# Performance work log

Hardware: AMD Instinct MI355X
Metric: run time of the kernel (lower is better)

The kernel has to match this reference:

```python
import jax, jax.numpy as jnp
import numpy as np

B, L, V, E_ENC, D_DEC, E_EMB = 256, 128, 4096, 1024, 1024, 512


def _lin(key, out_f, in_f, scale=0.02):
    k1, k2 = jax.random.split(key)
    return (jax.random.normal(k1, (out_f, in_f), jnp.float32) * scale,
            jax.random.normal(k2, (out_f,), jnp.float32) * scale)


def setup_inputs() -> dict:
    key = jax.random.key(0)
    ks = jax.random.split(key, 12)
    x = jax.random.normal(ks[0], (B, 1, V), jnp.float32)
    hidden = jax.random.normal(ks[1], (1, B, D_DEC), jnp.float32)
    enc_output = jax.random.normal(ks[2], (B, L, E_ENC), jnp.float32)
    W1_w, W1_b = _lin(ks[3], D_DEC, E_ENC)
    W2_w, W2_b = _lin(ks[4], D_DEC, D_DEC)
    V_w, V_b = _lin(ks[5], 1, D_DEC)
    out2emb_w, out2emb_b = _lin(ks[6], E_EMB, V)
    gru_wi, gru_bi = _lin(ks[7], 3 * D_DEC, E_EMB + E_ENC)
    gru_wh, gru_bh = _lin(ks[8], 3 * D_DEC, D_DEC)
    fc1_w, fc1_b = _lin(ks[9], E_EMB, D_DEC)
    fc2_w, fc2_b = _lin(ks[10], V, E_EMB)
    return dict(x=x, hidden=hidden, enc_output=enc_output,
                W1_w=W1_w, W1_b=W1_b, W2_w=W2_w, W2_b=W2_b, V_w=V_w, V_b=V_b,
                out2emb_w=out2emb_w, out2emb_b=out2emb_b,
                gru_wi=gru_wi, gru_wh=gru_wh, gru_bi=gru_bi, gru_bh=gru_bh,
                fc1_w=fc1_w, fc1_b=fc1_b, fc2_w=fc2_w, fc2_b=fc2_b)


def reference(x, hidden, enc_output, W1_w, W1_b, W2_w, W2_b, V_w, V_b,
              out2emb_w, out2emb_b, gru_wi, gru_wh, gru_bi, gru_bh,
              fc1_w, fc1_b, fc2_w, fc2_b):
    # --- Bahdanau additive attention ---
    h_t = hidden[-1][:, None, :]                                   # (B,1,dec)
    score = jnp.tanh(enc_output @ W1_w.T + W1_b + h_t @ W2_w.T + W2_b)  # (B,L,dec)
    attn = jax.nn.softmax(score @ V_w.T + V_b, axis=1)             # (B,L,1)
    context = jnp.sum(attn * enc_output, axis=1)                   # (B,enc)
    # --- embed previous output distribution ---
    x_emb = x @ out2emb_w.T + out2emb_b                            # (B,1,emb)
    rnn_in = jnp.concatenate([context[:, None, :], x_emb], -1)[:, 0, :]  # (B,emb+enc)
    # --- single GRU step (PyTorch gate layout r,z,n) ---
    h0 = hidden[0]
    gi = rnn_in @ gru_wi.T + gru_bi
    gh = h0 @ gru_wh.T + gru_bh
    ir, iz, inn = jnp.split(gi, 3, axis=-1)
    hr, hz, hn = jnp.split(gh, 3, axis=-1)
    r = jax.nn.sigmoid(ir + hr)
    z = jax.nn.sigmoid(iz + hz)
    n = jnp.tanh(inn + r * hn)
    h_new = (1.0 - z) * n + z * h0                                 # (B,dec)
    # --- output MLP ---
    out = jnp.tanh(h_new @ fc1_w.T + fc1_b) @ fc2_w.T + fc2_b      # (B,vocab)
    return out, h_new[None], attn
```

## Files before the change

kernel.cpp:

```cpp
#include <hip/hip_runtime.h>
#include <math.h>


#define B_   256
#define L_   128
#define V_   4096
#define ENC_ 1024
#define DEC_ 1024
#define EMB_ 512
#define MB_  1048576ull

typedef __bf16 bf16;
typedef __bf16 bf16x8 __attribute__((ext_vector_type(8)));
typedef __bf16 bf16x4 __attribute__((ext_vector_type(4)));
typedef float  f32x4  __attribute__((ext_vector_type(4)));

__device__ __forceinline__ float fast_tanh(float x) {
  float e = __builtin_amdgcn_exp2f(x * 2.88539008177792681472f);
  return 1.0f - 2.0f * __builtin_amdgcn_rcpf(e + 1.0f);
}
__device__ __forceinline__ float fast_sigmoid(float x) {
  return __builtin_amdgcn_rcpf(1.0f + __builtin_amdgcn_exp2f(-1.44269504088896f * x));
}

__device__ __forceinline__ void cp16(const void* g, void* l) {
  __builtin_amdgcn_global_load_lds(
      (const __attribute__((address_space(1))) void*)g,
      (__attribute__((address_space(3))) void*)l,
      16, 0, 0);
}

__device__ __forceinline__ bf16x8 ld8f(const float* f) {
  f32x4 a = *(const f32x4*)f;
  f32x4 b = *(const f32x4*)(f + 4);
  bf16x8 r;
  r[0] = (bf16)a[0]; r[1] = (bf16)a[1]; r[2] = (bf16)a[2]; r[3] = (bf16)a[3];
  r[4] = (bf16)b[0]; r[5] = (bf16)b[1]; r[6] = (bf16)b[2]; r[7] = (bf16)b[3];
  return r;
}


__device__ __forceinline__ void gemm64_f32(
    const float* __restrict__ A, const float* __restrict__ Brow,
    int strideA, int strideB, int kbeg, int kend, int row0,
    bf16* As, bf16* Bs, f32x4 acc[4])
{
  const int t   = threadIdx.x;
  const int lane = t & 63, w = t >> 6, q = lane >> 4, c16 = lane & 15;
  const int sr  = t >> 3, lb = t & 7;

  for (int k0 = kbeg; k0 < kend; k0 += 64) {
    bf16x8 va[2], vb[2];
#pragma unroll
    for (int ch = 0; ch < 2; ch++) {
      int r    = ch * 32 + sr;
      int gcol = k0 + ((lb ^ (r & 7)) << 3);
      va[ch] = ld8f(A    + (size_t)(row0 + r) * strideA + gcol);
      vb[ch] = ld8f(Brow + (size_t)r * strideB + gcol);
    }
#pragma unroll
    for (int ch = 0; ch < 2; ch++) {
      *(bf16x8*)&As[ch * 2048 + t * 8] = va[ch];
      *(bf16x8*)&Bs[ch * 2048 + t * 8] = vb[ch];
    }
    __syncthreads();
#pragma unroll
    for (int kkb = 0; kkb < 8; kkb += 4) {
      int rb = w * 16 + c16;
      bf16x8 bfr = *(const bf16x8*)&Bs[rb * 64 + (((kkb + q) ^ (rb & 7)) << 3)];
#pragma unroll
      for (int i = 0; i < 4; i++) {
        int ra = i * 16 + c16;
        bf16x8 af = *(const bf16x8*)&As[ra * 64 + (((kkb + q) ^ (ra & 7)) << 3)];
        acc[i] = __builtin_amdgcn_mfma_f32_16x16x32_bf16(af, bfr, acc[i], 0, 0, 0);
      }
    }
    __syncthreads();
  }
}

__global__ __launch_bounds__(256) void setup_k(
    const float* __restrict__ hidden, const float* __restrict__ W2,
    const float* __restrict__ wh, const float* __restrict__ W1_b,
    const float* __restrict__ W2_b, const float* __restrict__ gbh,
    const float* __restrict__ x, const float* __restrict__ o2e,
    const float* __restrict__ enc, const float* __restrict__ W1,
    const float* __restrict__ wi, const float* __restrict__ fc1w,
    const float* __restrict__ fc2w,
    bf16* __restrict__ enc_bf, bf16* __restrict__ W1_bf,
    bf16* __restrict__ wi_bf, bf16* __restrict__ fc1_bf,
    bf16* __restrict__ fc2_bf,
    bf16* __restrict__ u, bf16* __restrict__ gh, float* __restrict__ xe4)
{
  __shared__ __align__(16) bf16 As[64 * 64];
  __shared__ __align__(16) bf16 Bs[64 * 64];

  const int bid = blockIdx.x;
  const int t   = threadIdx.x;

  if (bid >= 384) {
    int i = bid - 384;
    const float* src; bf16* dst; int blk;
    if      (i < 8192) { src = enc;  dst = enc_bf; blk = i; }
    else if (i < 8448) { src = W1;   dst = W1_bf;  blk = i - 8192; }
    else if (i < 9600) { src = wi;   dst = wi_bf;  blk = i - 8448; }
    else if (i < 9728) { src = fc1w; dst = fc1_bf; blk = i - 9600; }
    else               { src = fc2w; dst = fc2_bf; blk = i - 9728; }
    const size_t base = (size_t)blk * 4096 + t * 16;
    const float* s = src + base;
    bf16* d = dst + base;
    *(bf16x8*)(d)     = ld8f(s);
    *(bf16x8*)(d + 8) = ld8f(s + 8);
    return;
  }

  const int lane = t & 63, w = t >> 6, q = lane >> 4, c16 = lane & 15;
  f32x4 acc[4] = {};

  if (bid < 256) {
    const int row0 = (bid >> 6) * 64;
    const int col0 = (bid & 63) * 64;
    const bool isU = (col0 < 1024);
    const float* Brow = isU ? (W2 + (size_t)col0 * 1024)
                            : (wh + (size_t)(col0 - 1024) * 1024);
    gemm64_f32(hidden, Brow, 1024, 1024, 0, 1024, row0, As, Bs, acc);

    const int gc = col0 + w * 16 + c16;
    float bias = isU ? (W1_b[gc] + W2_b[gc]) : gbh[gc - 1024];
#pragma unroll
    for (int i = 0; i < 4; i++) {
      int gr0 = row0 + i * 16 + q * 4;
#pragma unroll
      for (int r = 0; r < 4; r++) {
        float v = acc[i][r] + bias;
        if (isU) u[(size_t)(gr0 + r) * 1024 + gc] = (bf16)v;
        else     gh[(size_t)(gr0 + r) * 3072 + (gc - 1024)] = (bf16)v;
      }
    }
  } else {
    const int i3   = bid - 256;
    const int col0 = (i3 & 7) * 64;
    const int row0 = ((i3 >> 3) & 3) * 64;
    const int z    = i3 >> 5;
    gemm64_f32(x, o2e + (size_t)col0 * 4096, 4096, 4096,
               z * 1024, z * 1024 + 1024, row0, As, Bs, acc);

    const int gc = col0 + w * 16 + c16;
    float* out = xe4 + (size_t)z * 131072;
#pragma unroll
    for (int i = 0; i < 4; i++) {
      int gr0 = row0 + i * 16 + q * 4;
#pragma unroll
      for (int r = 0; r < 4; r++)
        out[(size_t)(gr0 + r) * 512 + gc] = acc[i][r];
    }
  }
}

__global__ __launch_bounds__(256) void score_f2(
    const bf16* __restrict__ A,
    const bf16* __restrict__ Bw,
    const bf16* __restrict__ u,
    const float* __restrict__ Vw,
    float* __restrict__ e_part)
{
  __shared__ __align__(16) bf16 As[128 * 64];
  __shared__ __align__(16) bf16 Bs[128 * 64];
  __shared__ float s_part[2][128];

  const int t    = threadIdx.x;
  const int lane = t & 63;
  const int w    = t >> 6;
  const int wm   = w >> 1;
  const int wn   = w & 1;
  const int q    = lane >> 4;
  const int c16  = lane & 15;
  const int sr   = t >> 3;
  const int lb   = t & 7;

  const int row0 = blockIdx.y * 128;
  const int b    = blockIdx.y;

  float rowsum[4][4] = {};

#pragma unroll 1
  for (int cbp = 0; cbp < 2; cbp++) {
    const int col0 = (blockIdx.x * 2 + cbp) * 128;
    f32x4 acc[4][4] = {};

    for (int k0 = 0; k0 < 1024; k0 += 64) {
#pragma unroll
      for (int ch = 0; ch < 4; ch++) {
        int r    = ch * 32 + sr;
        int gcol = k0 + ((lb ^ (r & 7)) << 3);
        cp16(A  + (size_t)(row0 + r) * 1024 + gcol, &As[ch * 2048 + t * 8]);
        cp16(Bw + (size_t)(col0 + r) * 1024 + gcol, &Bs[ch * 2048 + t * 8]);
      }
      __syncthreads();
#pragma unroll
      for (int kkb = 0; kkb < 8; kkb += 4) {
        bf16x8 af[4], bfr[4];
#pragma unroll
        for (int i = 0; i < 4; i++) {
          int ra = wm * 64 + i * 16 + c16;
          af[i] = *(const bf16x8*)&As[ra * 64 + (((kkb + q) ^ (ra & 7)) << 3)];
        }
#pragma unroll
        for (int j = 0; j < 4; j++) {
          int rb = wn * 64 + j * 16 + c16;
          bfr[j] = *(const bf16x8*)&Bs[rb * 64 + (((kkb + q) ^ (rb & 7)) << 3)];
        }
#pragma unroll
        for (int i = 0; i < 4; i++)
#pragma unroll
          for (int j = 0; j < 4; j++)
            acc[i][j] = __builtin_amdgcn_mfma_f32_16x16x32_bf16(af[i], bfr[j], acc[i][j], 0, 0, 0);
      }
      __syncthreads();
    }

#pragma unroll
    for (int i = 0; i < 4; i++) {
#pragma unroll
      for (int j = 0; j < 4; j++) {
        int gc   = col0 + wn * 64 + j * 16 + c16;
        float uc = (float)u[b * 1024 + gc];
        float vw = Vw[gc];
#pragma unroll
        for (int r = 0; r < 4; r++)
          rowsum[i][r] += fast_tanh(acc[i][j][r] + uc) * vw;
      }
    }
  }

#pragma unroll
  for (int i = 0; i < 4; i++) {
#pragma unroll
    for (int r = 0; r < 4; r++) {
      float v = rowsum[i][r];
      v += __shfl_xor(v, 1);
      v += __shfl_xor(v, 2);
      v += __shfl_xor(v, 4);
      v += __shfl_xor(v, 8);
      if (c16 == 0) s_part[wn][wm * 64 + i * 16 + q * 4 + r] = v;
    }
  }
  __syncthreads();
  if (t < 128)
    e_part[(size_t)blockIdx.x * 32768 + row0 + t] = s_part[0][t] + s_part[1][t];
}

__global__ __launch_bounds__(256) void softmax_f(
    const float* __restrict__ e_part,
    const bf16* __restrict__ enc,
    const float* __restrict__ xe4,
    const float* __restrict__ o2eb,
    float* __restrict__ attn_out,
    bf16* __restrict__ rnn_in)
{
  const int b = blockIdx.x;
  const int t = threadIdx.x;
  __shared__ float se[128];

  if (t < 128) {
    float s = 0.0f;
#pragma unroll
    for (int cb = 0; cb < 4; cb++) s += e_part[(size_t)cb * 32768 + b * 128 + t];
    se[t] = s;
  }
  __syncthreads();

  float m = -1e30f;
  for (int l = 0; l < 128; l++) m = fmaxf(m, se[l]);
  float sum = 0.0f;
  for (int l = 0; l < 128; l++) sum += expf(se[l] - m);
  float inv = 1.0f / sum;
  __syncthreads();
  if (t < 128) {
    float p = expf(se[t] - m) * inv;
    attn_out[b * 128 + t] = p;
    se[t] = p;
  }
  __syncthreads();

  float a0 = 0, a1 = 0, a2 = 0, a3 = 0;
  const bf16* ep = enc + (size_t)b * L_ * ENC_ + t * 4;
  for (int l = 0; l < 128; l++) {
    float p = se[l];
    bf16x4 v = *(const bf16x4*)(ep + (size_t)l * ENC_);
    a0 += p * (float)v[0]; a1 += p * (float)v[1];
    a2 += p * (float)v[2]; a3 += p * (float)v[3];
  }
  bf16x4 o;
  o[0] = (bf16)a0; o[1] = (bf16)a1; o[2] = (bf16)a2; o[3] = (bf16)a3;
  *(bf16x4*)(rnn_in + (size_t)b * 1536 + t * 4) = o;

#pragma unroll
  for (int jj = 0; jj < 2; jj++) {
    int j = jj * 256 + t;
    float v = o2eb[j];
#pragma unroll
    for (int z = 0; z < 4; z++) v += xe4[(size_t)z * 131072 + b * 512 + j];
    rnn_in[(size_t)b * 1536 + 1024 + j] = (bf16)v;
  }
}

template <int ACT, int OUTF32>
__global__ __launch_bounds__(256) void gemm_f(
    const bf16* __restrict__ A, const bf16* __restrict__ Bw,
    const float* __restrict__ bias1,
    void* __restrict__ C, int K, int out_ld)
{
  __shared__ __align__(16) bf16 As[64 * 64];
  __shared__ __align__(16) bf16 Bs[64 * 64];

  const int t    = threadIdx.x;
  const int lane = t & 63;
  const int w    = t >> 6;
  const int q    = lane >> 4;
  const int c16  = lane & 15;
  const int sr   = t >> 3;
  const int lb   = t & 7;
  const int row0 = blockIdx.y * 64;
  const int col0 = blockIdx.x * 64;

  f32x4 acc[4] = {};

  for (int k0 = 0; k0 < K; k0 += 64) {
#pragma unroll
    for (int ch = 0; ch < 2; ch++) {
      int r    = ch * 32 + sr;
      int gcol = k0 + ((lb ^ (r & 7)) << 3);
      cp16(A  + (size_t)(row0 + r) * K + gcol, &As[ch * 2048 + t * 8]);
      cp16(Bw + (size_t)(col0 + r) * K + gcol, &Bs[ch * 2048 + t * 8]);
    }
    __syncthreads();
#pragma unroll
    for (int kkb = 0; kkb < 8; kkb += 4) {
      int rb = w * 16 + c16;
      bf16x8 bfr = *(const bf16x8*)&Bs[rb * 64 + (((kkb + q) ^ (rb & 7)) << 3)];
#pragma unroll
      for (int i = 0; i < 4; i++) {
        int ra = i * 16 + c16;
        bf16x8 af = *(const bf16x8*)&As[ra * 64 + (((kkb + q) ^ (ra & 7)) << 3)];
        acc[i] = __builtin_amdgcn_mfma_f32_16x16x32_bf16(af, bfr, acc[i], 0, 0, 0);
      }
    }
    __syncthreads();
  }

  const int gc = col0 + w * 16 + c16;
  float bias = bias1[gc];
#pragma unroll
  for (int i = 0; i < 4; i++) {
    int gr0 = row0 + i * 16 + q * 4;
#pragma unroll
    for (int r = 0; r < 4; r++) {
      float v = acc[i][r] + bias;
      if (ACT == 1) v = fast_tanh(v);
      size_t off = (size_t)(gr0 + r) * out_ld + gc;
      if (OUTF32) ((float*)C)[off] = v;
      else        ((bf16*)C)[off] = (bf16)v;
    }
  }
}

__global__ __launch_bounds__(256) void gru_f(
    const bf16* __restrict__ gi, const bf16* __restrict__ gh,
    const float* __restrict__ h0,
    float* __restrict__ hnew_out, bf16* __restrict__ hnew_i)
{
  int idx = blockIdx.x * 256 + threadIdx.x;
  int b = idx >> 10, d = idx & 1023;
  const bf16* gib = gi + b * 3072;
  const bf16* ghb = gh + b * 3072;
  float ir = (float)gib[d], iz = (float)gib[1024 + d], in = (float)gib[2048 + d];
  float hr = (float)ghb[d], hz = (float)ghb[1024 + d], hn = (float)ghb[2048 + d];
  float r = fast_sigmoid(ir + hr);
  float z = fast_sigmoid(iz + hz);
  float n = fast_tanh(in + r * hn);
  float h = (1.0f - z) * n + z * h0[idx];
  hnew_out[idx] = h;
  hnew_i[idx]   = (bf16)h;
}

extern "C" void kernel_launch(void* const* d_in, const int* in_sizes, int n_in,
                              void* d_out, int out_size, void* d_ws, size_t ws_size,
                              hipStream_t stream) {
  const float* x      = (const float*)d_in[0];
  const float* hidden = (const float*)d_in[1];
  const float* enc    = (const float*)d_in[2];
  const float* W1_w   = (const float*)d_in[3];
  const float* W1_b   = (const float*)d_in[4];
  const float* W2_w   = (const float*)d_in[5];
  const float* W2_b   = (const float*)d_in[6];
  const float* V_w    = (const float*)d_in[7];
  const float* o2e_w  = (const float*)d_in[9];
  const float* o2e_b  = (const float*)d_in[10];
  const float* gru_wi = (const float*)d_in[11];
  const float* gru_wh = (const float*)d_in[12];
  const float* gru_bi = (const float*)d_in[13];
  const float* gru_bh = (const float*)d_in[14];
  const float* fc1_w  = (const float*)d_in[15];
  const float* fc1_b  = (const float*)d_in[16];
  const float* fc2_w  = (const float*)d_in[17];
  const float* fc2_b  = (const float*)d_in[18];

  float* out_main = (float*)d_out;
  float* out_h    = out_main + (size_t)B_ * V_;
  float* out_attn = out_h + (size_t)B_ * DEC_;

  char* ws = (char*)d_ws;
  bf16*  enc_bf  = (bf16*)(ws);
  bf16*  W1_bf   = (bf16*)(ws + 64 * MB_);
  bf16*  wi_bf   = (bf16*)(ws + 66 * MB_);
  bf16*  fc1_bf  = (bf16*)(ws + 75 * MB_);
  bf16*  fc2_bf  = (bf16*)(ws + 76 * MB_);
  bf16*  u_bf    = (bf16*)(ws + 80 * MB_);
  bf16*  gh_bf   = (bf16*)(ws + 80 * MB_ + 524288);
  float* e_part  = (float*)(ws + 82 * MB_);
  bf16*  gi_bf   = (bf16*)(ws + 82 * MB_ + 524288);
  bf16*  rnn_in  = (bf16*)(ws + 84 * MB_);
  bf16*  tbuf    = (bf16*)(ws + 84 * MB_ + 786432);
  bf16*  hnew_bf = (bf16*)(ws + 85 * MB_);
  float* xe4     = (float*)(ws + 85 * MB_ + 524288);

  setup_k<<<10624, 256, 0, stream>>>(
      hidden, W2_w, gru_wh, W1_b, W2_b, gru_bh, x, o2e_w,
      enc, W1_w, gru_wi, fc1_w, fc2_w,
      enc_bf, W1_bf, wi_bf, fc1_bf, fc2_bf, u_bf, gh_bf, xe4);

  score_f2<<<dim3(4, 256), 256, 0, stream>>>(enc_bf, W1_bf, u_bf, V_w, e_part);

  softmax_f<<<B_, 256, 0, stream>>>(e_part, enc_bf, xe4, o2e_b, out_attn, rnn_in);

  gemm_f<0, 0><<<dim3(48, 4), 256, 0, stream>>>(rnn_in, wi_bf, gru_bi, gi_bf, 1536, 3072);

  gru_f<<<(B_ * DEC_) / 256, 256, 0, stream>>>(gi_bf, gh_bf, hidden, out_h, hnew_bf);

  gemm_f<1, 0><<<dim3(8, 4), 256, 0, stream>>>(hnew_bf, fc1_bf, fc1_b, tbuf, 1024, 512);

  gemm_f<0, 1><<<dim3(64, 4), 256, 0, stream>>>(tbuf, fc2_bf, fc2_b, out_main, 512, 4096);
}
```

Baseline: 433.0 us.

## Fuse attention, softmax, GRU and output MLP into one persistent kernel with grid barriers

```diff
diff --git a/kernel.cpp b/kernel.cpp
--- a/kernel.cpp
+++ b/kernel.cpp
@@ -9,6 +9,7 @@
 #define DEC_ 1024
 #define EMB_ 512
 #define MB_  1048576ull
+#define NBLK 512
 
 typedef __bf16 bf16;
 typedef __bf16 bf16x8 __attribute__((ext_vector_type(8)));
@@ -39,16 +40,56 @@
   return r;
 }
 
+__device__ __forceinline__ void gbar(int* bar, int idx, int n) {
+  __syncthreads();
+  if (threadIdx.x == 0) {
+    __hip_atomic_fetch_add(&bar[idx], 1, __ATOMIC_ACQ_REL, __HIP_MEMORY_SCOPE_AGENT);
+    while (__hip_atomic_load(&bar[idx], __ATOMIC_ACQUIRE, __HIP_MEMORY_SCOPE_AGENT) < n)
+      __builtin_amdgcn_s_sleep(1);
+  }
+  __syncthreads();
+}
+
+
+__device__ __forceinline__ void gemm64_bf(
+    const bf16* __restrict__ A, const bf16* __restrict__ Bw, int K,
+    int row0, int col0, bf16* As, bf16* Bs, f32x4 acc[4])
+{
+  const int t = threadIdx.x;
+  const int lane = t & 63, w = t >> 6, q = lane >> 4, c16 = lane & 15;
+  const int sr = t >> 3, lb = t & 7;
+  for (int k0 = 0; k0 < K; k0 += 64) {
+#pragma unroll
+    for (int ch = 0; ch < 2; ch++) {
+      int r    = ch * 32 + sr;
+      int gcol = k0 + ((lb ^ (r & 7)) << 3);
+      cp16(A  + (size_t)(row0 + r) * K + gcol, &As[ch * 2048 + t * 8]);
+      cp16(Bw + (size_t)(col0 + r) * K + gcol, &Bs[ch * 2048 + t * 8]);
+    }
+    __syncthreads();
+#pragma unroll
+    for (int kkb = 0; kkb < 8; kkb += 4) {
+      int rb = w * 16 + c16;
+      bf16x8 bfr = *(const bf16x8*)&Bs[rb * 64 + (((kkb + q) ^ (rb & 7)) << 3)];
+#pragma unroll
+      for (int i = 0; i < 4; i++) {
+        int ra = i * 16 + c16;
+        bf16x8 af = *(const bf16x8*)&As[ra * 64 + (((kkb + q) ^ (ra & 7)) << 3)];
+        acc[i] = __builtin_amdgcn_mfma_f32_16x16x32_bf16(af, bfr, acc[i], 0, 0, 0);
+      }
+    }
+    __syncthreads();
+  }
+}
 
 __device__ __forceinline__ void gemm64_f32(
     const float* __restrict__ A, const float* __restrict__ Brow,
     int strideA, int strideB, int kbeg, int kend, int row0,
     bf16* As, bf16* Bs, f32x4 acc[4])
 {
-  const int t   = threadIdx.x;
+  const int t = threadIdx.x;
   const int lane = t & 63, w = t >> 6, q = lane >> 4, c16 = lane & 15;
-  const int sr  = t >> 3, lb = t & 7;
-
+  const int sr = t >> 3, lb = t & 7;
   for (int k0 = kbeg; k0 < kend; k0 += 64) {
     bf16x8 va[2], vb[2];
 #pragma unroll
@@ -157,17 +198,25 @@
   }
 }
 
-__global__ __launch_bounds__(256) void score_f2(
-    const bf16* __restrict__ A,
-    const bf16* __restrict__ Bw,
-    const bf16* __restrict__ u,
-    const float* __restrict__ Vw,
-    float* __restrict__ e_part)
+__global__ __launch_bounds__(256) void mega_k(
+    const bf16* __restrict__ enc_bf, const bf16* __restrict__ W1_bf,
+    const bf16* __restrict__ u_bf, const float* __restrict__ Vw,
+    float* __restrict__ e_part,
+    const float* __restrict__ xe4, const float* __restrict__ o2eb,
+    const bf16* __restrict__ wi_bf, const float* __restrict__ gru_bi,
+    const bf16* __restrict__ gh_bf, const float* __restrict__ h0,
+    const bf16* __restrict__ fc1_bf, const float* __restrict__ fc1_b,
+    const bf16* __restrict__ fc2_bf, const float* __restrict__ fc2_b,
+    bf16* __restrict__ rnn_in, bf16* __restrict__ gi_bf,
+    bf16* __restrict__ hnew_bf, bf16* __restrict__ tbuf,
+    float* __restrict__ attn_out, float* __restrict__ out_h,
+    float* __restrict__ out_main, int* __restrict__ bar)
 {
   __shared__ __align__(16) bf16 As[128 * 64];
   __shared__ __align__(16) bf16 Bs[128 * 64];
-  __shared__ float s_part[2][128];
-
+  __shared__ float s_misc[256];
+
+  const int bid  = blockIdx.x;
   const int t    = threadIdx.x;
   const int lane = t & 63;
   const int w    = t >> 6;
@@ -178,210 +227,193 @@
   const int sr   = t >> 3;
   const int lb   = t & 7;
 
-  const int row0 = blockIdx.y * 128;
-  const int b    = blockIdx.y;
-
-  float rowsum[4][4] = {};
+  {
+    const int b    = bid >> 1;
+    const int half = bid & 1;
+    const int row0 = b * 128;
+    float rowsum[4][4] = {};
 
 #pragma unroll 1
-  for (int cbp = 0; cbp < 2; cbp++) {
-    const int col0 = (blockIdx.x * 2 + cbp) * 128;
-    f32x4 acc[4][4] = {};
-
-    for (int k0 = 0; k0 < 1024; k0 += 64) {
-#pragma unroll
-      for (int ch = 0; ch < 4; ch++) {
-        int r    = ch * 32 + sr;
-        int gcol = k0 + ((lb ^ (r & 7)) << 3);
-        cp16(A  + (size_t)(row0 + r) * 1024 + gcol, &As[ch * 2048 + t * 8]);
-        cp16(Bw + (size_t)(col0 + r) * 1024 + gcol, &Bs[ch * 2048 + t * 8]);
+    for (int cb = half * 4; cb < half * 4 + 4; cb++) {
+      const int col0 = cb * 128;
+      f32x4 acc[4][4] = {};
+
+      for (int k0 = 0; k0 < 1024; k0 += 64) {
+#pragma unroll
+        for (int ch = 0; ch < 4; ch++) {
+          int r    = ch * 32 + sr;
+          int gcol = k0 + ((lb ^ (r & 7)) << 3);
+          cp16(enc_bf + (size_t)(row0 + r) * 1024 + gcol, &As[ch * 2048 + t * 8]);
+          cp16(W1_bf  + (size_t)(col0 + r) * 1024 + gcol, &Bs[ch * 2048 + t * 8]);
+        }
+        __syncthreads();
+#pragma unroll
+        for (int kkb = 0; kkb < 8; kkb += 4) {
+          bf16x8 af[4], bfr[4];
+#pragma unroll
+          for (int i = 0; i < 4; i++) {
+            int ra = wm * 64 + i * 16 + c16;
+            af[i] = *(const bf16x8*)&As[ra * 64 + (((kkb + q) ^ (ra & 7)) << 3)];
+          }
+#pragma unroll
+          for (int j = 0; j < 4; j++) {
+            int rb = wn * 64 + j * 16 + c16;
+            bfr[j] = *(const bf16x8*)&Bs[rb * 64 + (((kkb + q) ^ (rb & 7)) << 3)];
+          }
+#pragma unroll
+          for (int i = 0; i < 4; i++)
+#pragma unroll
+            for (int j = 0; j < 4; j++)
+              acc[i][j] = __builtin_amdgcn_mfma_f32_16x16x32_bf16(af[i], bfr[j], acc[i][j], 0, 0, 0);
+        }
+        __syncthreads();
       }
-      __syncthreads();
-#pragma unroll
-      for (int kkb = 0; kkb < 8; kkb += 4) {
-        bf16x8 af[4], bfr[4];
-#pragma unroll
-        for (int i = 0; i < 4; i++) {
-          int ra = wm * 64 + i * 16 + c16;
-          af[i] = *(const bf16x8*)&As[ra * 64 + (((kkb + q) ^ (ra & 7)) << 3)];
+
+#pragma unroll
+      for (int i = 0; i < 4; i++)
+#pragma unroll
+        for (int j = 0; j < 4; j++) {
+          int gc   = col0 + wn * 64 + j * 16 + c16;
+          float uc = (float)u_bf[b * 1024 + gc];
+          float vw = Vw[gc];
+#pragma unroll
+          for (int r = 0; r < 4; r++)
+            rowsum[i][r] += fast_tanh(acc[i][j][r] + uc) * vw;
         }
-#pragma unroll
-        for (int j = 0; j < 4; j++) {
-          int rb = wn * 64 + j * 16 + c16;
-          bfr[j] = *(const bf16x8*)&Bs[rb * 64 + (((kkb + q) ^ (rb & 7)) << 3)];
-        }
-#pragma unroll
-        for (int i = 0; i < 4; i++)
-#pragma unroll
-          for (int j = 0; j < 4; j++)
-            acc[i][j] = __builtin_amdgcn_mfma_f32_16x16x32_bf16(af[i], bfr[j], acc[i][j], 0, 0, 0);
+    }
+
+#pragma unroll
+    for (int i = 0; i < 4; i++)
+#pragma unroll
+      for (int r = 0; r < 4; r++) {
+        float v = rowsum[i][r];
+        v += __shfl_xor(v, 1);
+        v += __shfl_xor(v, 2);
+        v += __shfl_xor(v, 4);
+        v += __shfl_xor(v, 8);
+        if (c16 == 0) s_misc[wn * 128 + wm * 64 + i * 16 + q * 4 + r] = v;
       }
-      __syncthreads();
-    }
-
+    __syncthreads();
+    if (t < 128)
+      e_part[(size_t)half * 32768 + row0 + t] = s_misc[t] + s_misc[128 + t];
+  }
+
+  gbar(bar, 0, NBLK);
+
+  if ((bid & 1) == 0) {
+    const int b = bid >> 1;
+    if (t < 128)
+      s_misc[t] = e_part[b * 128 + t] + e_part[32768 + b * 128 + t];
+    __syncthreads();
+
+    float m = -1e30f;
+    for (int l = 0; l < 128; l++) m = fmaxf(m, s_misc[l]);
+    float sum = 0.0f;
+    for (int l = 0; l < 128; l++) sum += expf(s_misc[l] - m);
+    float inv = 1.0f / sum;
+    __syncthreads();
+    if (t < 128) {
+      float p = expf(s_misc[t] - m) * inv;
+      attn_out[b * 128 + t] = p;
+      s_misc[t] = p;
+    }
+    __syncthreads();
+
+    float a0 = 0, a1 = 0, a2 = 0, a3 = 0;
+    const bf16* ep = enc_bf + (size_t)b * L_ * ENC_ + t * 4;
+    for (int l = 0; l < 128; l++) {
+      float p = s_misc[l];
+      bf16x4 v = *(const bf16x4*)(ep + (size_t)l * ENC_);
+      a0 += p * (float)v[0]; a1 += p * (float)v[1];
+      a2 += p * (float)v[2]; a3 += p * (float)v[3];
+    }
+    bf16x4 o;
+    o[0] = (bf16)a0; o[1] = (bf16)a1; o[2] = (bf16)a2; o[3] = (bf16)a3;
+    *(bf16x4*)(rnn_in + (size_t)b * 1536 + t * 4) = o;
+
+#pragma unroll
+    for (int jj = 0; jj < 2; jj++) {
+      int j = jj * 256 + t;
+      float v = o2eb[j];
+#pragma unroll
+      for (int z = 0; z < 4; z++) v += xe4[(size_t)z * 131072 + b * 512 + j];
+      rnn_in[(size_t)b * 1536 + 1024 + j] = (bf16)v;
+    }
+  }
+
+  gbar(bar, 1, NBLK);
+
+  if (bid < 192) {
+    const int col0 = (bid % 48) * 64;
+    const int row0 = (bid / 48) * 64;
+    f32x4 acc[4] = {};
+    gemm64_bf(rnn_in, wi_bf, 1536, row0, col0, As, Bs, acc);
+    const int gc = col0 + w * 16 + c16;
+    float bias = gru_bi[gc];
 #pragma unroll
     for (int i = 0; i < 4; i++) {
-#pragma unroll
-      for (int j = 0; j < 4; j++) {
-        int gc   = col0 + wn * 64 + j * 16 + c16;
-        float uc = (float)u[b * 1024 + gc];
-        float vw = Vw[gc];
-#pragma unroll
-        for (int r = 0; r < 4; r++)
-          rowsum[i][r] += fast_tanh(acc[i][j][r] + uc) * vw;
-      }
-    }
-  }
-
-#pragma unroll
-  for (int i = 0; i < 4; i++) {
-#pragma unroll
-    for (int r = 0; r < 4; r++) {
-      float v = rowsum[i][r];
-      v += __shfl_xor(v, 1);
-      v += __shfl_xor(v, 2);
-      v += __shfl_xor(v, 4);
-      v += __shfl_xor(v, 8);
-      if (c16 == 0) s_part[wn][wm * 64 + i * 16 + q * 4 + r] = v;
-    }
-  }
-  __syncthreads();
-  if (t < 128)
-    e_part[(size_t)blockIdx.x * 32768 + row0 + t] = s_part[0][t] + s_part[1][t];
-}
-
-__global__ __launch_bounds__(256) void softmax_f(
-    const float* __restrict__ e_part,
-    const bf16* __restrict__ enc,
-    const float* __restrict__ xe4,
-    const float* __restrict__ o2eb,
-    float* __restrict__ attn_out,
-    bf16* __restrict__ rnn_in)
-{
-  const int b = blockIdx.x;
-  const int t = threadIdx.x;
-  __shared__ float se[128];
-
-  if (t < 128) {
-    float s = 0.0f;
-#pragma unroll
-    for (int cb = 0; cb < 4; cb++) s += e_part[(size_t)cb * 32768 + b * 128 + t];
-    se[t] = s;
-  }
-  __syncthreads();
-
-  float m = -1e30f;
-  for (int l = 0; l < 128; l++) m = fmaxf(m, se[l]);
-  float sum = 0.0f;
-  for (int l = 0; l < 128; l++) sum += expf(se[l] - m);
-  float inv = 1.0f / sum;
-  __syncthreads();
-  if (t < 128) {
-    float p = expf(se[t] - m) * inv;
-    attn_out[b * 128 + t] = p;
-    se[t] = p;
-  }
-  __syncthreads();
-
-  float a0 = 0, a1 = 0, a2 = 0, a3 = 0;
-  const bf16* ep = enc + (size_t)b * L_ * ENC_ + t * 4;
-  for (int l = 0; l < 128; l++) {
-    float p = se[l];
-    bf16x4 v = *(const bf16x4*)(ep + (size_t)l * ENC_);
-    a0 += p * (float)v[0]; a1 += p * (float)v[1];
-    a2 += p * (float)v[2]; a3 += p * (float)v[3];
-  }
-  bf16x4 o;
-  o[0] = (bf16)a0; o[1] = (bf16)a1; o[2] = (bf16)a2; o[3] = (bf16)a3;
-  *(bf16x4*)(rnn_in + (size_t)b * 1536 + t * 4) = o;
-
-#pragma unroll
-  for (int jj = 0; jj < 2; jj++) {
-    int j = jj * 256 + t;
-    float v = o2eb[j];
-#pragma unroll
-    for (int z = 0; z < 4; z++) v += xe4[(size_t)z * 131072 + b * 512 + j];
-    rnn_in[(size_t)b * 1536 + 1024 + j] = (bf16)v;
-  }
-}
-
-template <int ACT, int OUTF32>
-__global__ __launch_bounds__(256) void gemm_f(
-    const bf16* __restrict__ A, const bf16* __restrict__ Bw,
-    const float* __restrict__ bias1,
-    void* __restrict__ C, int K, int out_ld)
-{
-  __shared__ __align__(16) bf16 As[64 * 64];
-  __shared__ __align__(16) bf16 Bs[64 * 64];
-
-  const int t    = threadIdx.x;
-  const int lane = t & 63;
-  const int w    = t >> 6;
-  const int q    = lane >> 4;
-  const int c16  = lane & 15;
-  const int sr   = t >> 3;
-  const int lb   = t & 7;
-  const int row0 = blockIdx.y * 64;
-  const int col0 = blockIdx.x * 64;
-
-  f32x4 acc[4] = {};
-
-  for (int k0 = 0; k0 < K; k0 += 64) {
-#pragma unroll
-    for (int ch = 0; ch < 2; ch++) {
-      int r    = ch * 32 + sr;
-      int gcol = k0 + ((lb ^ (r & 7)) << 3);
-      cp16(A  + (size_t)(row0 + r) * K + gcol, &As[ch * 2048 + t * 8]);
-      cp16(Bw + (size_t)(col0 + r) * K + gcol, &Bs[ch * 2048 + t * 8]);
-    }
-    __syncthreads();
-#pragma unroll
-    for (int kkb = 0; kkb < 8; kkb += 4) {
-      int rb = w * 16 + c16;
-      bf16x8 bfr = *(const bf16x8*)&Bs[rb * 64 + (((kkb + q) ^ (rb & 7)) << 3)];
-#pragma unroll
-      for (int i = 0; i < 4; i++) {
-        int ra = i * 16 + c16;
-        bf16x8 af = *(const bf16x8*)&As[ra * 64 + (((kkb + q) ^ (ra & 7)) << 3)];
-        acc[i] = __builtin_amdgcn_mfma_f32_16x16x32_bf16(af, bfr, acc[i], 0, 0, 0);
-      }
-    }
-    __syncthreads();
-  }
-
-  const int gc = col0 + w * 16 + c16;
-  float bias = bias1[gc];
-#pragma unroll
-  for (int i = 0; i < 4; i++) {
-    int gr0 = row0 + i * 16 + q * 4;
-#pragma unroll
-    for (int r = 0; r < 4; r++) {
-      float v = acc[i][r] + bias;
-      if (ACT == 1) v = fast_tanh(v);
-      size_t off = (size_t)(gr0 + r) * out_ld + gc;
-      if (OUTF32) ((float*)C)[off] = v;
-      else        ((bf16*)C)[off] = (bf16)v;
-    }
-  }
-}
-
-__global__ __launch_bounds__(256) void gru_f(
-    const bf16* __restrict__ gi, const bf16* __restrict__ gh,
-    const float* __restrict__ h0,
-    float* __restrict__ hnew_out, bf16* __restrict__ hnew_i)
-{
-  int idx = blockIdx.x * 256 + threadIdx.x;
-  int b = idx >> 10, d = idx & 1023;
-  const bf16* gib = gi + b * 3072;
-  const bf16* ghb = gh + b * 3072;
-  float ir = (float)gib[d], iz = (float)gib[1024 + d], in = (float)gib[2048 + d];
-  float hr = (float)ghb[d], hz = (float)ghb[1024 + d], hn = (float)ghb[2048 + d];
-  float r = fast_sigmoid(ir + hr);
-  float z = fast_sigmoid(iz + hz);
-  float n = fast_tanh(in + r * hn);
-  float h = (1.0f - z) * n + z * h0[idx];
-  hnew_out[idx] = h;
-  hnew_i[idx]   = (bf16)h;
+      int gr0 = row0 + i * 16 + q * 4;
+#pragma unroll
+      for (int r = 0; r < 4; r++)
+        gi_bf[(size_t)(gr0 + r) * 3072 + gc] = (bf16)(acc[i][r] + bias);
+    }
+  }
+
+  gbar(bar, 2, NBLK);
+
+  if ((bid & 1) == 0) {
+    const int b = bid >> 1;
+    const bf16* gib = gi_bf + (size_t)b * 3072;
+    const bf16* ghb = gh_bf + (size_t)b * 3072;
+#pragma unroll
+    for (int k = 0; k < 4; k++) {
+      int d = t + k * 256;
+      float ir = (float)gib[d], iz = (float)gib[1024 + d], in = (float)gib[2048 + d];
+      float hr = (float)ghb[d], hz = (float)ghb[1024 + d], hn = (float)ghb[2048 + d];
+      float r = fast_sigmoid(ir + hr);
+      float z = fast_sigmoid(iz + hz);
+      float n = fast_tanh(in + r * hn);
+      float h = (1.0f - z) * n + z * h0[(size_t)b * 1024 + d];
+      out_h[(size_t)b * 1024 + d] = h;
+      hnew_bf[(size_t)b * 1024 + d] = (bf16)h;
+    }
+  }
+
+  gbar(bar, 3, NBLK);
+
+  if (bid < 32) {
+    const int col0 = (bid % 8) * 64;
+    const int row0 = (bid / 8) * 64;
+    f32x4 acc[4] = {};
+    gemm64_bf(hnew_bf, fc1_bf, 1024, row0, col0, As, Bs, acc);
+    const int gc = col0 + w * 16 + c16;
+    float bias = fc1_b[gc];
+#pragma unroll
+    for (int i = 0; i < 4; i++) {
+      int gr0 = row0 + i * 16 + q * 4;
+#pragma unroll
+      for (int r = 0; r < 4; r++)
+        tbuf[(size_t)(gr0 + r) * 512 + gc] = (bf16)fast_tanh(acc[i][r] + bias);
+    }
+  }
+
+  gbar(bar, 4, NBLK);
+
+  if (bid < 256) {
+    const int col0 = (bid % 64) * 64;
+    const int row0 = (bid / 64) * 64;
+    f32x4 acc[4] = {};
+    gemm64_bf(tbuf, fc2_bf, 512, row0, col0, As, Bs, acc);
+    const int gc = col0 + w * 16 + c16;
+    float bias = fc2_b[gc];
+#pragma unroll
+    for (int i = 0; i < 4; i++) {
+      int gr0 = row0 + i * 16 + q * 4;
+#pragma unroll
+      for (int r = 0; r < 4; r++)
+        out_main[(size_t)(gr0 + r) * 4096 + gc] = acc[i][r] + bias;
+    }
+  }
 }
 
 extern "C" void kernel_launch(void* const* d_in, const int* in_sizes, int n_in,
@@ -424,21 +456,17 @@
   bf16*  tbuf    = (bf16*)(ws + 84 * MB_ + 786432);
   bf16*  hnew_bf = (bf16*)(ws + 85 * MB_);
   float* xe4     = (float*)(ws + 85 * MB_ + 524288);
+  int*   bar     = (int*)(ws + 88 * MB_);
+
+  hipMemsetAsync(bar, 0, 16 * sizeof(int), stream);
 
   setup_k<<<10624, 256, 0, stream>>>(
       hidden, W2_w, gru_wh, W1_b, W2_b, gru_bh, x, o2e_w,
       enc, W1_w, gru_wi, fc1_w, fc2_w,
       enc_bf, W1_bf, wi_bf, fc1_bf, fc2_bf, u_bf, gh_bf, xe4);
 
-  score_f2<<<dim3(4, 256), 256, 0, stream>>>(enc_bf, W1_bf, u_bf, V_w, e_part);
-
-  softmax_f<<<B_, 256, 0, stream>>>(e_part, enc_bf, xe4, o2e_b, out_attn, rnn_in);
-
-  gemm_f<0, 0><<<dim3(48, 4), 256, 0, stream>>>(rnn_in, wi_bf, gru_bi, gi_bf, 1536, 3072);
-
-  gru_f<<<(B_ * DEC_) / 256, 256, 0, stream>>>(gi_bf, gh_bf, hidden, out_h, hnew_bf);
-
-  gemm_f<1, 0><<<dim3(8, 4), 256, 0, stream>>>(hnew_bf, fc1_bf, fc1_b, tbuf, 1024, 512);
-
-  gemm_f<0, 1><<<dim3(64, 4), 256, 0, stream>>>(tbuf, fc2_bf, fc2_b, out_main, 512, 4096);
-}
+  mega_k<<<NBLK, 256, 0, stream>>>(
+      enc_bf, W1_bf, u_bf, V_w, e_part, xe4, o2e_b,
+      wi_bf, gru_bi, gh_bf, hidden, fc1_bf, fc1_b, fc2_bf, fc2_b,
+      rnn_in, gi_bf, hnew_bf, tbuf, out_attn, out_h, out_main, bar);
+}
```

Result: slower. 754.3 us (+74.2%).
